# Performance work log

Measured on AMD Instinct MI355X. Metric: run time of the kernel, lower is better.

## Reference

```python
import jax, jax.numpy as jnp
from jax import lax
import numpy as np

T, B, D, H = 2048, 32, 256, 256

def setup_inputs() -> dict:
    key = jax.random.key(0)
    ks = jax.random.split(key, 8)
    inp = {
        'input_': jax.random.normal(ks[0], (T, B, D), dtype=jnp.float32),
        'length': jax.random.randint(ks[1], (B,), 0, T, dtype=jnp.int64),
        'Wih0': jax.random.normal(ks[2], (D, 3 * H), dtype=jnp.float32) * 0.05,
        'Whh0': jax.random.normal(ks[3], (H, 3 * H), dtype=jnp.float32) * 0.05,
        'b0': jax.random.normal(ks[4], (3 * H,), dtype=jnp.float32) * 0.05,
        'Wih1': jax.random.normal(ks[5], (H, 3 * H), dtype=jnp.float32) * 0.05,
        'Whh1': jax.random.normal(ks[6], (H, 3 * H), dtype=jnp.float32) * 0.05,
        'b1': jax.random.normal(ks[7], (3 * H,), dtype=jnp.float32) * 0.05,
    }
    return inp


def _run_layer(x, length, Wih, Whh, b, h0):
    # x: [T, B, D_in]; scan over time with hidden state carried on-chip.
    def step(h, xs):
        x_t, t_idx = xs
        pre = h @ Whh + x_t @ Wih + b          # [B, 3H]
        h_pre, t_pre, _c_pre = jnp.split(pre, 3, axis=1)
        t_gate = jax.nn.sigmoid(t_pre)
        c_gate = jax.nn.sigmoid(t_gate)         # bug-faithful: sigmoid of sigmoid(t_pre)
        s_t = jnp.tanh(h_pre) * t_gate + h * c_gate
        mask = (t_idx < length)[:, None]         # [B, 1]
        h_next = jnp.where(mask, s_t, h)
        return h_next, h_next
    times = jnp.arange(x.shape[0])
    h_n, out = lax.scan(step, h0, (x, times))
    return out, h_n


def reference(input_, length, Wih0, Whh0, b0, Wih1, Whh1, b1):
    h0 = jnp.zeros((input_.shape[1], H), dtype=input_.dtype)
    out0, hn0 = _run_layer(input_, length, Wih0, Whh0, b0, h0)
    # dropout=0 -> identity between layers; each layer reuses the same zero h_0
    out1, hn1 = _run_layer(out0, length, Wih1, Whh1, b1, h0)
    h_n = jnp.stack([hn0, hn1], axis=0)          # [num_layers, B, H]
    return out1, h_n
```

## Files before the change

### kernel.cpp

```cpp
#include <hip/hip_runtime.h>
#include <cstdint>
#include <cstddef>

static constexpr int T_STEPS = 2048;
static constexpr int BATCH   = 32;
static constexpr int DIM     = 256;
static constexpr int NCOL    = 512;
static constexpr size_t M_ROWS = (size_t)T_STEPS * BATCH;

typedef _Float16 f16x4 __attribute__((ext_vector_type(4)));
typedef _Float16 f16x8 __attribute__((ext_vector_type(8)));
typedef float    f32x4 __attribute__((ext_vector_type(4)));
struct alignas(8) H4 { _Float16 x, y, z, w; };

static constexpr size_t XW_OFF   = 0;
static constexpr size_t A_OFF    = M_ROWS * NCOL * 2;
static constexpr size_t BLOB_OFF = A_OFF + M_ROWS * DIM * 2;
static constexpr size_t BLOB_ELT = (size_t)DIM * NCOL;
static constexpr size_t FLAG_OFF = BLOB_OFF + 4 * BLOB_ELT * 2;

__global__ void cvt_f32_to_f16(const float* __restrict__ src, _Float16* __restrict__ dst,
                               int n4, int* __restrict__ flags) {
  if (blockIdx.x == 0 && threadIdx.x < BATCH) flags[threadIdx.x] = 0;
  int i = blockIdx.x * blockDim.x + threadIdx.x;
  if (i >= n4) return;
  float4 v = ((const float4*)src)[i];
  H4 o; o.x = (_Float16)v.x; o.y = (_Float16)v.y; o.z = (_Float16)v.z; o.w = (_Float16)v.w;
  ((H4*)dst)[i] = o;
}

__global__ void prep_blobs4(const float* __restrict__ w0, const float* __restrict__ w1,
                            const float* __restrict__ w2, const float* __restrict__ w3,
                            _Float16* __restrict__ blobs) {
  int gid = blockIdx.x * blockDim.x + threadIdx.x;
  int mat = gid >> 17;
  int rem = gid & 131071;
  int k = rem >> 9;
  int n = rem & 511;
  const float* src = (mat == 0) ? w0 : (mat == 1) ? w1 : (mat == 2) ? w2 : w3;
  float v = src[k * 768 + n];
  int kc = k >> 5, q = (k >> 3) & 3, j = k & 7, tn = n >> 4;
  int lane = (n & 15) + 16 * q;
  blobs[(size_t)mat * BLOB_ELT + ((size_t)(tn * 8 + kc) * 64 + lane) * 8 + j] = (_Float16)v;
}

__global__ __launch_bounds__(256) void gemm_xw(const _Float16* __restrict__ A,
                                               const _Float16* __restrict__ blob,
                                               const float* __restrict__ bias,
                                               _Float16* __restrict__ XW) {
  int lane = threadIdx.x & 63;
  int wave = threadIdx.x >> 6;
  int wid  = blockIdx.x * 4 + wave;
  int mbase = (wid >> 1) * 16;
  int nhalf = wid & 1;
  int q = lane >> 4, n15 = lane & 15;

  f32x4 acc[16];
#pragma unroll
  for (int i = 0; i < 16; i++) acc[i] = (f32x4){0.f, 0.f, 0.f, 0.f};

  const _Float16* Arow = A + (size_t)(mbase + n15) * DIM + q * 8;
#pragma unroll
  for (int kc = 0; kc < 8; kc++) {
    f16x8 af = *(const f16x8*)(Arow + kc * 32);
#pragma unroll
    for (int nt = 0; nt < 16; nt++) {
      const _Float16* bp = blob + ((size_t)((nhalf * 16 + nt) * 8 + kc) * 64 + lane) * 8;
      f16x8 bf = *(const f16x8*)bp;
      acc[nt] = __builtin_amdgcn_mfma_f32_16x16x32_f16(af, bf, acc[nt], 0, 0, 0);
    }
  }
#pragma unroll
  for (int nt = 0; nt < 16; nt++) {
    int col = nhalf * 256 + nt * 16 + n15;
    float bv = bias[col];
#pragma unroll
    for (int r = 0; r < 4; r++) {
      int m = mbase + q * 4 + r;
      XW[(size_t)m * NCOL + col] = (_Float16)(acc[nt][r] + bv);
    }
  }
}

__device__ __forceinline__ int read_len(const void* p, int b) {
  const long long* q = (const long long*)p;
  bool ok64 = true;
  for (int i = 0; i < 32; i++) { long long v = q[i]; if (v < 0 || v > 2048) ok64 = false; }
  return ok64 ? (int)q[b] : ((const int*)p)[b];
}

__device__ __forceinline__ void gload_lds_row(const _Float16* g, _Float16* l) {
  __builtin_amdgcn_global_load_lds(
      (const __attribute__((address_space(1))) void*)g,
      (__attribute__((address_space(3))) void*)l, 16, 0, 0);
}

__device__ __forceinline__ void gate_update(float pre_h, float pre_t, bool live, float& h) {
  const float K1 = 1.442695040888963f, K2 = 2.885390081777927f;
  float phc = fminf(fmaxf(pre_h, -20.f), 20.f);
  float e1 = __builtin_amdgcn_exp2f(-K2 * phc);
  float e2 = __builtin_amdgcn_exp2f(-K1 * pre_t);
  float u1 = 1.f + e1;
  float rr = __builtin_amdgcn_rcpf(u1 * (1.f + e2));
  float ttg = (1.f - e1) * rr;
  float tg  = u1 * rr;
  float cg = 0.5f + tg * (0.250905f + tg * (-0.00432f + tg * (-0.015525f)));
  float s = ttg + h * cg;
  h = live ? s : h;
}

__global__ __launch_bounds__(512, 2) void recur_fused(const _Float16* __restrict__ xw0,
                                                      const _Float16* __restrict__ bwhh0,
                                                      const _Float16* __restrict__ bwhh1,
                                                      const _Float16* __restrict__ bwih1,
                                                      const float* __restrict__ b1,
                                                      const void* __restrict__ lenp,
                                                      _Float16* __restrict__ out0,
                                                      float* __restrict__ out1,
                                                      float* __restrict__ hn,
                                                      int* __restrict__ flags) {
  const int bid  = blockIdx.x;
  const int tid  = threadIdx.x;
  const int w    = tid >> 6;
  const int lane = tid & 63;
  const int q = lane >> 4, l15 = lane & 15;

  __shared__ __align__(16) _Float16 hbuf[2][DIM];
  __shared__ __align__(16) _Float16 xbuf[2][16][NCOL];

  const int c0 = (2 * w) * 16 + l15;
  const int c1 = (2 * w + 1) * 16 + l15;

  if (bid < BATCH) {
    const int b = bid;
    const int len = read_len(lenp, b);
    f16x8 Bh[2][8], Bt[2][8];
#pragma unroll
    for (int pp = 0; pp < 2; pp++)
#pragma unroll
      for (int kc = 0; kc < 8; kc++) {
        Bh[pp][kc] = *(const f16x8*)(bwhh0 + ((size_t)((2 * w + pp) * 8 + kc) * 64 + lane) * 8);
        Bt[pp][kc] = *(const f16x8*)(bwhh0 + ((size_t)((16 + 2 * w + pp) * 8 + kc) * 64 + lane) * 8);
      }
    if (tid < DIM) hbuf[0][tid] = (_Float16)0.f;

    const _Float16* xrow = xw0 + (size_t)b * NCOL;
    const size_t xstride = (size_t)BATCH * NCOL;

    gload_lds_row(xrow + (size_t)(2 * w)     * xstride + lane * 8, &xbuf[0][2 * w][0]);
    gload_lds_row(xrow + (size_t)(2 * w + 1) * xstride + lane * 8, &xbuf[0][2 * w + 1][0]);
    asm volatile("s_waitcnt vmcnt(0)" ::: "memory");
    __syncthreads();

    float h0 = 0.f, h1 = 0.f;
    for (int tb = 0; tb < T_STEPS / 16; ++tb) {
      const int buf = tb & 1;
      if (tb + 1 < T_STEPS / 16) {
        const _Float16* gsrc = xrow + (size_t)((tb + 1) * 16) * xstride;
        gload_lds_row(gsrc + (size_t)(2 * w)     * xstride + lane * 8, &xbuf[1 - buf][2 * w][0]);
        gload_lds_row(gsrc + (size_t)(2 * w + 1) * xstride + lane * 8, &xbuf[1 - buf][2 * w + 1][0]);
      }
#pragma unroll
      for (int ts = 0; ts < 16; ++ts) {
        const int t = tb * 16 + ts;
        const int p = ts & 1;
        const _Float16* xr = &xbuf[buf][ts][0];
        const float xh0 = (float)xr[c0],       xh1 = (float)xr[c1];
        const float xt0 = (float)xr[c0 + 256], xt1 = (float)xr[c1 + 256];

        f32x4 a0 = {0.f, 0.f, 0.f, 0.f}, a1 = a0, a2 = a0, a3 = a0;
        const _Float16* hb = &hbuf[p][q * 8];
#pragma unroll
        for (int kc = 0; kc < 8; kc++) {
          f16x8 a = *(const f16x8*)(hb + kc * 32);
          a0 = __builtin_amdgcn_mfma_f32_16x16x32_f16(a, Bh[0][kc], a0, 0, 0, 0);
          a1 = __builtin_amdgcn_mfma_f32_16x16x32_f16(a, Bh[1][kc], a1, 0, 0, 0);
          a2 = __builtin_amdgcn_mfma_f32_16x16x32_f16(a, Bt[0][kc], a2, 0, 0, 0);
          a3 = __builtin_amdgcn_mfma_f32_16x16x32_f16(a, Bt[1][kc], a3, 0, 0, 0);
        }
        const bool live = t < len;
        gate_update(a0[0] + xh0, a2[0] + xt0, live, h0);
        gate_update(a1[0] + xh1, a3[0] + xt1, live, h1);
        _Float16 s0 = (_Float16)h0, s1 = (_Float16)h1;
        if (q == 0) {
          hbuf[1 - p][c0] = s0;
          hbuf[1 - p][c1] = s1;
          size_t o = ((size_t)t * BATCH + b) * DIM;
          out0[o + c0] = s0; out0[o + c1] = s1;
        }
        if (ts == 15) {
          asm volatile("s_waitcnt vmcnt(0) lgkmcnt(0)\n\ts_barrier" ::: "memory");
        } else {
          asm volatile("s_waitcnt lgkmcnt(0)\n\ts_barrier" ::: "memory");
        }
      }
      if (tid == 0)
        __hip_atomic_store(&flags[b], tb + 1, __ATOMIC_RELEASE, __HIP_MEMORY_SCOPE_AGENT);
    }
    if (q == 0) {
      hn[b * DIM + c0] = h0;
      hn[b * DIM + c1] = h1;
    }
  } else {
    const int b = bid - BATCH;
    const int len = read_len(lenp, b);
    f16x8 Bh[2][8], Bt[2][8];
#pragma unroll
    for (int pp = 0; pp < 2; pp++)
#pragma unroll
      for (int kc = 0; kc < 8; kc++) {
        Bh[pp][kc] = *(const f16x8*)(bwhh1 + ((size_t)((2 * w + pp) * 8 + kc) * 64 + lane) * 8);
        Bt[pp][kc] = *(const f16x8*)(bwhh1 + ((size_t)((16 + 2 * w + pp) * 8 + kc) * 64 + lane) * 8);
      }
    const float bb0 = b1[c0], bb1 = b1[c1], bb2 = b1[c0 + 256], bb3 = b1[c1 + 256];
    if (tid < DIM) hbuf[0][tid] = (_Float16)0.f;
    __syncthreads();

    float h0 = 0.f, h1 = 0.f;
    for (int tb = 0; tb < T_STEPS / 16; ++tb) {
      if (tid == 0) {
        int it = 0;
        while (__hip_atomic_load(&flags[b], __ATOMIC_RELAXED, __HIP_MEMORY_SCOPE_AGENT) <= tb) {
          __builtin_amdgcn_s_sleep(2);
          if (++it > (1 << 20)) break;
        }
        (void)__hip_atomic_load(&flags[b], __ATOMIC_ACQUIRE, __HIP_MEMORY_SCOPE_AGENT);
      }
      __syncthreads();

      const int t0 = tb * 16;
      const _Float16* arow = out0 + ((size_t)(t0 + l15) * BATCH + b) * DIM + q * 8;
      f16x8 xa[8];
#pragma unroll
      for (int kc = 0; kc < 8; kc++) xa[kc] = *(const f16x8*)(arow + kc * 32);
#pragma unroll
      for (int ti = 0; ti < 4; ti++) {
        const int tn  = (ti < 2) ? (2 * w + ti) : (16 + 2 * w + (ti - 2));
        f32x4 acc = {0.f, 0.f, 0.f, 0.f};
#pragma unroll
        for (int kc = 0; kc < 8; kc++) {
          f16x8 bf = *(const f16x8*)(bwih1 + ((size_t)(tn * 8 + kc) * 64 + lane) * 8);
          acc = __builtin_amdgcn_mfma_f32_16x16x32_f16(xa[kc], bf, acc, 0, 0, 0);
        }
        const int   col = (ti == 0) ? c0 : (ti == 1) ? c1 : (ti == 2) ? (c0 + 256) : (c1 + 256);
        const float bv  = (ti == 0) ? bb0 : (ti == 1) ? bb1 : (ti == 2) ? bb2 : bb3;
#pragma unroll
        for (int r = 0; r < 4; r++) xbuf[0][q * 4 + r][col] = (_Float16)(acc[r] + bv);
      }
      asm volatile("s_waitcnt lgkmcnt(0)\n\ts_barrier" ::: "memory");

#pragma unroll
      for (int ts = 0; ts < 16; ++ts) {
        const int t = t0 + ts;
        const int p = ts & 1;
        const _Float16* xr = &xbuf[0][ts][0];
        const float xh0 = (float)xr[c0],       xh1 = (float)xr[c1];
        const float xt0 = (float)xr[c0 + 256], xt1 = (float)xr[c1 + 256];

        f32x4 a0 = {0.f, 0.f, 0.f, 0.f}, a1 = a0, a2 = a0, a3 = a0;
        const _Float16* hb = &hbuf[p][q * 8];
#pragma unroll
        for (int kc = 0; kc < 8; kc++) {
          f16x8 a = *(const f16x8*)(hb + kc * 32);
          a0 = __builtin_amdgcn_mfma_f32_16x16x32_f16(a, Bh[0][kc], a0, 0, 0, 0);
          a1 = __builtin_amdgcn_mfma_f32_16x16x32_f16(a, Bh[1][kc], a1, 0, 0, 0);
          a2 = __builtin_amdgcn_mfma_f32_16x16x32_f16(a, Bt[0][kc], a2, 0, 0, 0);
          a3 = __builtin_amdgcn_mfma_f32_16x16x32_f16(a, Bt[1][kc], a3, 0, 0, 0);
        }
        const bool live = t < len;
        gate_update(a0[0] + xh0, a2[0] + xt0, live, h0);
        gate_update(a1[0] + xh1, a3[0] + xt1, live, h1);
        if (q == 0) {
          hbuf[1 - p][c0] = (_Float16)h0;
          hbuf[1 - p][c1] = (_Float16)h1;
          size_t o = ((size_t)t * BATCH + b) * DIM;
          out1[o + c0] = h0; out1[o + c1] = h1;
        }
        asm volatile("s_waitcnt lgkmcnt(0)\n\ts_barrier" ::: "memory");
      }
    }
    if (q == 0) {
      hn[BATCH * DIM + b * DIM + c0] = h0;
      hn[BATCH * DIM + b * DIM + c1] = h1;
    }
  }
}

extern "C" void kernel_launch(void* const* d_in, const int* in_sizes, int n_in,
                              void* d_out, int out_size, void* d_ws, size_t ws_size,
                              hipStream_t stream) {
  const float* input_ = (const float*)d_in[0];
  const void*  lenp   = d_in[1];
  const float* Wih0   = (const float*)d_in[2];
  const float* Whh0   = (const float*)d_in[3];
  const float* b0     = (const float*)d_in[4];
  const float* Wih1   = (const float*)d_in[5];
  const float* Whh1   = (const float*)d_in[6];
  const float* b1     = (const float*)d_in[7];
  float* out = (float*)d_out;
  char*  ws  = (char*)d_ws;

  _Float16* XW    = (_Float16*)(ws + XW_OFF);
  _Float16* Abuf  = (_Float16*)(ws + A_OFF);
  _Float16* blobs = (_Float16*)(ws + BLOB_OFF);
  int*      flags = (int*)(ws + FLAG_OFF);
  float* hn = out + M_ROWS * DIM;

  cvt_f32_to_f16<<<16384, 256, 0, stream>>>(input_, Abuf, (int)(M_ROWS * DIM / 4), flags);
  prep_blobs4<<<2048, 256, 0, stream>>>(Wih0, Wih1, Whh0, Whh1, blobs);
  gemm_xw<<<2048, 256, 0, stream>>>(Abuf, blobs + 0 * BLOB_ELT, b0, XW);
  recur_fused<<<2 * BATCH, 512, 0, stream>>>(XW,
                                             blobs + 2 * BLOB_ELT,
                                             blobs + 3 * BLOB_ELT,
                                             blobs + 1 * BLOB_ELT,
                                             b1, lenp, Abuf, out, hn, flags);
}
```

Before: 2.525 ms.

## Double-buffer layer-1 input projection to overlap with recurrence

Layer-1 blocks now prefetch the next 16-step chunk of layer-0 output and compute its input-projection GEMM into a second LDS buffer after finishing the current chunk's recurrence. Previously the block waited on the flag, loaded and projected the chunk, and only then started the serial steps. The wait now runs one chunk ahead, so global-load latency and the flag handshake can overlap with the 16 recurrent steps. In exchange, every lane now spins on the flag instead of only thread 0, the consumer must lag the producer by an extra chunk, and the spin limit is raised.

```diff
diff --git a/kernel.cpp b/kernel.cpp
--- a/kernel.cpp
+++ b/kernel.cpp
@@ -130,6 +130,7 @@
 
   const int c0 = (2 * w) * 16 + l15;
   const int c1 = (2 * w + 1) * 16 + l15;
+  constexpr int NB = T_STEPS / 16;
 
   if (bid < BATCH) {
     const int b = bid;
@@ -153,9 +154,9 @@
     __syncthreads();
 
     float h0 = 0.f, h1 = 0.f;
-    for (int tb = 0; tb < T_STEPS / 16; ++tb) {
+    for (int tb = 0; tb < NB; ++tb) {
       const int buf = tb & 1;
-      if (tb + 1 < T_STEPS / 16) {
+      if (tb + 1 < NB) {
         const _Float16* gsrc = xrow + (size_t)((tb + 1) * 16) * xstride;
         gload_lds_row(gsrc + (size_t)(2 * w)     * xstride + lane * 8, &xbuf[1 - buf][2 * w][0]);
         gload_lds_row(gsrc + (size_t)(2 * w + 1) * xstride + lane * 8, &xbuf[1 - buf][2 * w + 1][0]);
@@ -216,44 +217,63 @@
     if (tid < DIM) hbuf[0][tid] = (_Float16)0.f;
     __syncthreads();
 
+#define WAIT_FLAG(TH_)                                                                   \
+    {                                                                                    \
+      int it = 0;                                                                        \
+      while (__hip_atomic_load(&flags[b], __ATOMIC_RELAXED, __HIP_MEMORY_SCOPE_AGENT)    \
+             < (TH_)) {                                                                  \
+        __builtin_amdgcn_s_sleep(2);                                                     \
+        if (++it > (1 << 22)) break;           \
+      }                                                                                  \
+      (void)__hip_atomic_load(&flags[b], __ATOMIC_ACQUIRE, __HIP_MEMORY_SCOPE_AGENT);    \
+    }
+
+#define XGEMM(XA_, DST_)                                                                 \
+    {                                                                                    \
+      _Pragma("unroll")                                                                  \
+      for (int ti = 0; ti < 4; ti++) {                                                   \
+        const int tn = (ti < 2) ? (2 * w + ti) : (16 + 2 * w + (ti - 2));                \
+        f32x4 acc = {0.f, 0.f, 0.f, 0.f};                                                \
+        _Pragma("unroll")                                                                \
+        for (int kc = 0; kc < 8; kc++) {                                                 \
+          f16x8 bf = *(const f16x8*)(bwih1 + ((size_t)(tn * 8 + kc) * 64 + lane) * 8);   \
+          acc = __builtin_amdgcn_mfma_f32_16x16x32_f16(XA_[kc], bf, acc, 0, 0, 0);       \
+        }                                                                                \
+        const int   col = (ti == 0) ? c0 : (ti == 1) ? c1 : (ti == 2) ? (c0 + 256)       \
+                                                                      : (c1 + 256);      \
+        const float bv  = (ti == 0) ? bb0 : (ti == 1) ? bb1 : (ti == 2) ? bb2 : bb3;     \
+        _Pragma("unroll")                                                                \
+        for (int r = 0; r < 4; r++) xbuf[DST_][q * 4 + r][col] = (_Float16)(acc[r] + bv);\
+      }                                                                                  \
+    }
+
     float h0 = 0.f, h1 = 0.f;
-    for (int tb = 0; tb < T_STEPS / 16; ++tb) {
-      if (tid == 0) {
-        int it = 0;
-        while (__hip_atomic_load(&flags[b], __ATOMIC_RELAXED, __HIP_MEMORY_SCOPE_AGENT) <= tb) {
-          __builtin_amdgcn_s_sleep(2);
-          if (++it > (1 << 20)) break;
-        }
-        (void)__hip_atomic_load(&flags[b], __ATOMIC_ACQUIRE, __HIP_MEMORY_SCOPE_AGENT);
-      }
-      __syncthreads();
-
-      const int t0 = tb * 16;
-      const _Float16* arow = out0 + ((size_t)(t0 + l15) * BATCH + b) * DIM + q * 8;
-      f16x8 xa[8];
-#pragma unroll
-      for (int kc = 0; kc < 8; kc++) xa[kc] = *(const f16x8*)(arow + kc * 32);
-#pragma unroll
-      for (int ti = 0; ti < 4; ti++) {
-        const int tn  = (ti < 2) ? (2 * w + ti) : (16 + 2 * w + (ti - 2));
-        f32x4 acc = {0.f, 0.f, 0.f, 0.f};
-#pragma unroll
-        for (int kc = 0; kc < 8; kc++) {
-          f16x8 bf = *(const f16x8*)(bwih1 + ((size_t)(tn * 8 + kc) * 64 + lane) * 8);
-          acc = __builtin_amdgcn_mfma_f32_16x16x32_f16(xa[kc], bf, acc, 0, 0, 0);
-        }
-        const int   col = (ti == 0) ? c0 : (ti == 1) ? c1 : (ti == 2) ? (c0 + 256) : (c1 + 256);
-        const float bv  = (ti == 0) ? bb0 : (ti == 1) ? bb1 : (ti == 2) ? bb2 : bb3;
-#pragma unroll
-        for (int r = 0; r < 4; r++) xbuf[0][q * 4 + r][col] = (_Float16)(acc[r] + bv);
-      }
-      asm volatile("s_waitcnt lgkmcnt(0)\n\ts_barrier" ::: "memory");
-
+
+    WAIT_FLAG(1);
+    {
+      const _Float16* arow = out0 + ((size_t)l15 * BATCH + b) * DIM + q * 8;
+      f16x8 xa0[8];
+#pragma unroll
+      for (int kc = 0; kc < 8; kc++) xa0[kc] = *(const f16x8*)(arow + kc * 32);
+      XGEMM(xa0, 0);
+    }
+    asm volatile("s_waitcnt lgkmcnt(0)\n\ts_barrier" ::: "memory");
+
+    f16x8 xa[8];
+    for (int tb = 0; tb < NB; ++tb) {
+      const int buf = tb & 1;
+      if (tb + 1 < NB) {
+        WAIT_FLAG(tb + 2);
+        const _Float16* arow =
+            out0 + ((size_t)((tb + 1) * 16 + l15) * BATCH + b) * DIM + q * 8;
+#pragma unroll
+        for (int kc = 0; kc < 8; kc++) xa[kc] = *(const f16x8*)(arow + kc * 32);
+      }
 #pragma unroll
       for (int ts = 0; ts < 16; ++ts) {
-        const int t = t0 + ts;
+        const int t = tb * 16 + ts;
         const int p = ts & 1;
-        const _Float16* xr = &xbuf[0][ts][0];
+        const _Float16* xr = &xbuf[buf][ts][0];
         const float xh0 = (float)xr[c0],       xh1 = (float)xr[c1];
         const float xt0 = (float)xr[c0 + 256], xt1 = (float)xr[c1 + 256];
 
@@ -278,7 +298,13 @@
         }
         asm volatile("s_waitcnt lgkmcnt(0)\n\ts_barrier" ::: "memory");
       }
-    }
+      if (tb + 1 < NB) {
+        XGEMM(xa, 1 - buf);
+        asm volatile("s_waitcnt lgkmcnt(0)\n\ts_barrier" ::: "memory");
+      }
+    }
+#undef XGEMM
+#undef WAIT_FLAG
     if (q == 0) {
       hn[BATCH * DIM + b * DIM + c0] = h0;
       hn[BATCH * DIM + b * DIM + c1] = h1;
```

New measurement: 2.495 ms. About the same (-1.2%).
